# Kernel optimization log

Measured on AMD Instinct MI355X. Metric: run time of the kernel, lower is better.

The kernel has to match this reference:

```python
import jax, jax.numpy as jnp
import numpy as np
from jax import lax

GRAVITY = 9.8
DT = 0.1
MAX_STEPS = 200


def _conv(x, w, b):
    # x: [N,C,H,W], w: [O,I,3,3] (PyTorch OIHW), padding=1 -> SAME
    y = lax.conv_general_dilated(x, w, window_strides=(1, 1), padding='SAME',
                                 dimension_numbers=('NCHW', 'OIHW', 'NCHW'))
    return y + b[None, :, None, None]


def _maxpool2(x):
    return lax.reduce_window(x, -jnp.inf, lax.max,
                             window_dimensions=(1, 1, 2, 2),
                             window_strides=(1, 1, 2, 2), padding='VALID')


def setup_inputs() -> dict:
    key = jax.random.key(0)
    ks = jax.random.split(key, 12)
    B = 256
    x = jax.random.normal(ks[0], (B, 12, 128, 128), dtype=jnp.float32)

    def he(k, shape, fan_in):
        return jax.random.normal(k, shape, dtype=jnp.float32) * np.float32(np.sqrt(2.0 / fan_in))

    w1 = he(ks[1], (32, 12, 3, 3), 12 * 9); b1 = jnp.zeros((32,), jnp.float32)
    w2 = he(ks[2], (64, 32, 3, 3), 32 * 9); b2 = jnp.zeros((64,), jnp.float32)
    w3 = he(ks[3], (64, 64, 3, 3), 64 * 9); b3 = jnp.zeros((64,), jnp.float32)
    w4 = he(ks[4], (64, 64, 3, 3), 64 * 9); b4 = jnp.zeros((64,), jnp.float32)
    wl1 = he(ks[5], (128, 64 * 8 * 8), 64 * 8 * 8); bl1 = jnp.zeros((128,), jnp.float32)
    wl2 = he(ks[6], (4, 128), 128); bl2 = jnp.zeros((4,), jnp.float32)
    return {'x': x, 'w1': w1, 'b1': b1, 'w2': w2, 'b2': b2, 'w3': w3, 'b3': b3,
            'w4': w4, 'b4': b4, 'wl1': wl1, 'bl1': bl1, 'wl2': wl2, 'bl2': bl2}


def _forward(x, w1, b1, w2, b2, w3, b3, w4, b4, wl1, bl1, wl2, bl2):
    h = _maxpool2(jax.nn.relu(_conv(x, w1, b1)))   # [B,32,64,64]
    h = _maxpool2(jax.nn.relu(_conv(h, w2, b2)))   # [B,64,32,32]
    h = _maxpool2(jax.nn.relu(_conv(h, w3, b3)))   # [B,64,16,16]
    h = _maxpool2(jax.nn.relu(_conv(h, w4, b4)))   # [B,64,8,8]
    h = h.reshape(h.shape[0], -1)                  # [B,4096]
    h = jax.nn.relu(h @ wl1.T + bl1)               # [B,128]
    state = h @ wl2.T + bl2                        # [B,4]

    px, py, vx, vy = state[:, 0], state[:, 1], state[:, 2], state[:, 3]

    def step(carry, _):
        cx, cy, cvy = carry
        nvy = cvy - GRAVITY * DT
        nx = cx + vx * DT
        ny = jnp.maximum(cy + nvy * DT, 0.0)
        return (nx, ny, nvy), None

    (fx, _, _), _ = lax.scan(step, (px, py, vy), None, length=MAX_STEPS)
    return fx


def reference(x, w1, b1, w2, b2, w3, b3, w4, b4, wl1, bl1, wl2, bl2):
    return _forward(x, w1, b1, w2, b2, w3, b3, w4, b4, wl1, bl1, wl2, bl2)
```

## Files before the change

kernel.cpp:

```cpp
#include <hip/hip_runtime.h>


typedef _Float16 f16;
typedef _Float16 f16x8 __attribute__((ext_vector_type(8)));
typedef _Float16 f16x4 __attribute__((ext_vector_type(4)));
typedef float f32x4 __attribute__((ext_vector_type(4)));
typedef float f32x16 __attribute__((ext_vector_type(16)));

__global__ __launch_bounds__(512)
void pack_weights(const float* __restrict__ w1, const float* __restrict__ w2,
                  const float* __restrict__ w3, const float* __restrict__ w4,
                  f16* __restrict__ apack) {
  int idx = blockIdx.x * 512 + threadIdx.x;
  int frag = idx >> 9;
  int e = idx & 511;
  int lane = e >> 3, j = e & 7;
  float v = 0.f;
  if (frag < 9) {
    int kh = frag / 3, kw = frag % 3;
    int oc = lane & 31;
    int ic = (lane >> 5) * 8 + j;
    if (ic < 12) v = w1[((oc * 12 + ic) * 3 + kh) * 3 + kw];
  } else if (frag < 45) {
    int f = frag - 9;
    int sh = f >> 2, og = f & 3;
    int kh = sh / 3, kw = sh % 3;
    int row16 = lane & 15, kg = lane >> 4;
    int oc = og * 16 + row16;
    int ic = kg * 8 + j;
    v = w2[((oc * 32 + ic) * 3 + kh) * 3 + kw];
  } else {
    const float* w = (frag < 117) ? w3 : w4;
    int f = frag - ((frag < 117) ? 45 : 117);
    int sk = f >> 2, og = f & 3;
    int sh = sk >> 1, ks = sk & 1;
    int kh = sh / 3, kw = sh % 3;
    int row16 = lane & 15, kg = lane >> 4;
    int oc = og * 16 + row16;
    int ic = ks * 32 + kg * 8 + j;
    v = w[((oc * 64 + ic) * 3 + kh) * 3 + kw];
  }
  apack[idx] = (f16)v;
}

__global__ __launch_bounds__(512)
void conv1_mfma(const float* __restrict__ x, const f16* __restrict__ apack,
                const float* __restrict__ bias, f16* __restrict__ hout) {
  constexpr int W = 128, H = 128;
  constexpr int SR = 6, PADB = 48, ROWB = 130 * PADB;
  __shared__ char smem[SR * ROWB];
  const int tid = threadIdx.x;
  const int n = blockIdx.y;
  const int r0 = blockIdx.x * 4;

  if (tid < 36) {
    int slot = tid / 6, r = tid % 6;
    int px = (r >= 3) ? 129 : 0;
    int ch = r % 3;
    *(float4*)(smem + slot * ROWB + px * PADB + ch * 16) =
        make_float4(0.f, 0.f, 0.f, 0.f);
  }
  {
    const int g = tid >> 4;
    const int l16 = tid & 15;
    const int Q = l16 >> 2, q = l16 & 3;
    float4 a[SR];
#pragma unroll
    for (int sr = 0; sr < SR; ++sr) {
      const int ri = r0 + sr - 1;
      a[sr] = make_float4(0.f, 0.f, 0.f, 0.f);
      if (l16 < 12 && ri >= 0 && ri < H)
        a[sr] = *(const float4*)(x + ((size_t)(n * 12 + l16) * H + ri) * W + g * 4);
    }
#pragma unroll
    for (int sr = 0; sr < SR; ++sr) {
      float4 t1, t2;
      {
        float sx = __shfl_xor(a[sr].x, 1), sy = __shfl_xor(a[sr].y, 1);
        float sz = __shfl_xor(a[sr].z, 1), sw = __shfl_xor(a[sr].w, 1);
        bool odd = q & 1;
        t1.x = odd ? sy : a[sr].x;  t1.y = odd ? a[sr].y : sx;
        t1.z = odd ? sw : a[sr].z;  t1.w = odd ? a[sr].w : sz;
      }
      {
        float sx = __shfl_xor(t1.x, 2), sy = __shfl_xor(t1.y, 2);
        float sz = __shfl_xor(t1.z, 2), sw = __shfl_xor(t1.w, 2);
        bool hi = q & 2;
        t2.x = hi ? sz : t1.x;  t2.y = hi ? sw : t1.y;
        t2.z = hi ? t1.z : sx;  t2.w = hi ? t1.w : sy;
      }
      f16x4 h = { (f16)t2.x, (f16)t2.y, (f16)t2.z, (f16)t2.w };
      *(f16x4*)(smem + sr * ROWB + (g * 4 + q + 1) * PADB + Q * 8) = h;
    }
  }
  __syncthreads();

  const int wv = tid >> 6, l = tid & 63;
  const int rp = wv >> 2;
  const int pxb = (wv & 3) * 32;
  const int rl0 = rp * 2;
  const int ln = l & 31;
  const int hi = l >> 5;

  f16x8 A[9];
#pragma unroll
  for (int ks = 0; ks < 9; ++ks)
    A[ks] = *(const f16x8*)(apack + ((ks << 9) + (l << 3)));

  f32x16 acc[2];
  acc[0] = (f32x16)0.f;
  acc[1] = (f32x16)0.f;

#pragma unroll
  for (int rowi = 0; rowi < 2; ++rowi) {
#pragma unroll
    for (int ks = 0; ks < 9; ++ks) {
      const int kh = ks / 3, kw = ks % 3;
      const int slot = rl0 + rowi + kh;
      f16x8 B = *(const f16x8*)(smem + slot * ROWB + (pxb + ln + kw) * PADB + hi * 16);
      acc[rowi] = __builtin_amdgcn_mfma_f32_32x32x16_f16(A[ks], B, acc[rowi], 0, 0, 0);
    }
  }
  const int pr = blockIdx.x * 2 + rp;
#pragma unroll
  for (int g = 0; g < 4; ++g) {
    float v[4];
#pragma unroll
    for (int c = 0; c < 4; ++c) {
      float m = fmaxf(acc[0][g * 4 + c], acc[1][g * 4 + c]);
      v[c] = fmaxf(m, __shfl_xor(m, 1));
    }
    if ((l & 1) == 0) {
      const int pw = (pxb + ln) >> 1;
      const int oc0 = g * 8 + hi * 4;
      f16x4 pk;
#pragma unroll
      for (int c = 0; c < 4; ++c)
        pk[c] = (f16)fmaxf(v[c] + bias[oc0 + c], 0.f);
      *(f16x4*)(hout + (((size_t)(n * 64 + pr) * 64 + pw) * 32 + oc0)) = pk;
    }
  }
}

template<int C, int W, int H, int BR, int KS, int PADB, int PGn, bool NCHW_OUT>
__global__ __launch_bounds__(256)
void conv_shift(const f16* __restrict__ hin, const f16* __restrict__ apack,
                const float* __restrict__ bias, void* __restrict__ hout) {
  constexpr int SR = BR + 2;
  constexpr int ROWB = (W + 2) * PADB;
  __shared__ char smem[SR * ROWB];
  const int tid = threadIdx.x;
  const int n = blockIdx.y;
  const int r0 = blockIdx.x * BR;
  constexpr int CPC = C / 8;
  constexpr int TOTC = SR * (W + 2) * CPC;
  constexpr int NITER = (TOTC + 255) / 256;
  {
    float4 stg[NITER];
#pragma unroll
    for (int it = 0; it < NITER; ++it) {
      const int t = tid + it * 256;
      float4 v = make_float4(0.f, 0.f, 0.f, 0.f);
      if (t < TOTC) {
        int sr = t / ((W + 2) * CPC);
        int rem = t - sr * ((W + 2) * CPC);
        int px = rem / CPC;
        int kc = rem - px * CPC;
        int ri = r0 + sr - 1;
        int gx = px - 1;
        if (ri >= 0 && ri < H && gx >= 0 && gx < W)
          v = *(const float4*)(hin + (((size_t)(n * H + ri) * W + gx) * C + kc * 8));
      }
      stg[it] = v;
    }
#pragma unroll
    for (int it = 0; it < NITER; ++it) {
      const int t = tid + it * 256;
      if (t < TOTC) {
        int sr = t / ((W + 2) * CPC);
        int rem = t - sr * ((W + 2) * CPC);
        int px = rem / CPC;
        int kc = rem - px * CPC;
        *(float4*)(smem + sr * ROWB + px * PADB + kc * 16) = stg[it];
      }
    }
  }
  __syncthreads();

  const int wv = tid >> 6, l = tid & 63;
  constexpr int WPP = W / (16 * PGn);
  const int rp = wv / WPP;
  const int pxb = (wv % WPP) * 16 * PGn;
  const int rl0 = rp * 2;
  const int lp = l & 15, kg = l >> 4;
  const int px0 = pxb + lp;

  f32x4 acc[2][PGn][4];
#pragma unroll
  for (int a = 0; a < 2; ++a)
#pragma unroll
    for (int b = 0; b < PGn; ++b)
#pragma unroll
      for (int c = 0; c < 4; ++c)
        acc[a][b][c] = (f32x4){0.f, 0.f, 0.f, 0.f};

  for (int sh = 0; sh < 9; ++sh) {
    const int kh = sh / 3, kw = sh % 3;
    f16x8 A[KS][4];
#pragma unroll
    for (int ks = 0; ks < KS; ++ks)
#pragma unroll
      for (int og = 0; og < 4; ++og)
        A[ks][og] = *(const f16x8*)(apack + ((((sh * KS + ks) * 4 + og) << 9) + (l << 3)));
#pragma unroll
    for (int rowi = 0; rowi < 2; ++rowi) {
      const char* base = smem + (rl0 + rowi + kh) * ROWB;
#pragma unroll
      for (int pg = 0; pg < PGn; ++pg) {
#pragma unroll
        for (int ks = 0; ks < KS; ++ks) {
          f16x8 B = *(const f16x8*)(base + (px0 + pg * 16 + kw) * PADB + ks * 64 + kg * 16);
#pragma unroll
          for (int og = 0; og < 4; ++og)
            acc[rowi][pg][og] =
                __builtin_amdgcn_mfma_f32_16x16x32_f16(A[ks][og], B, acc[rowi][pg][og], 0, 0, 0);
        }
      }
    }
  }
  constexpr int PH = H / 2, PW = W / 2;
  const int pr = blockIdx.x * (BR / 2) + rp;
#pragma unroll
  for (int pg = 0; pg < PGn; ++pg) {
#pragma unroll
    for (int og = 0; og < 4; ++og) {
      float v[4];
#pragma unroll
      for (int c = 0; c < 4; ++c) {
        float m = fmaxf(acc[0][pg][og][c], acc[1][pg][og][c]);
        v[c] = fmaxf(m, __shfl_xor(m, 1));
      }
      if ((l & 1) == 0) {
        const int pw = (pxb + pg * 16 + lp) >> 1;
        const int oc0 = og * 16 + kg * 4;
        if constexpr (NCHW_OUT) {
          float* o = (float*)hout;
#pragma unroll
          for (int c = 0; c < 4; ++c)
            o[(((size_t)n * 64 + oc0 + c) * PH + pr) * PW + pw] =
                fmaxf(v[c] + bias[oc0 + c], 0.f);
        } else {
          f16x4 pk;
#pragma unroll
          for (int c = 0; c < 4; ++c)
            pk[c] = (f16)fmaxf(v[c] + bias[oc0 + c], 0.f);
          *(f16x4*)((f16*)hout + (((size_t)(n * PH + pr) * PW + pw) * 64 + oc0)) = pk;
        }
      }
    }
  }
}

__global__ __launch_bounds__(1024)
void fc_head(const float* __restrict__ h4, const float* __restrict__ wl1,
             const float* __restrict__ bl1, const float* __restrict__ wl2,
             const float* __restrict__ bl2, float* __restrict__ out) {
  __shared__ float rows[2][4096];
  __shared__ float red[8 * 128 * 2];
  __shared__ float red2[2 * 128];
  const int tid = threadIdx.x;
  const int b0 = blockIdx.x * 2;
  {
    const float4* src = (const float4*)(h4 + (size_t)b0 * 4096);
    float4* dst = (float4*)rows;
    for (int t = tid; t < 2048; t += 1024) dst[t] = src[t];
  }
  __syncthreads();

  const int nn = tid & 127;
  const int ks = tid >> 7;
  const float4* wp = (const float4*)(wl1 + (size_t)nn * 4096 + ks * 512);
  const float4* x0 = (const float4*)(&rows[0][ks * 512]);
  const float4* x1 = (const float4*)(&rows[1][ks * 512]);
  float s0 = 0.f, s1 = 0.f;
#pragma unroll 8
  for (int i = 0; i < 128; ++i) {
    float4 w = wp[i], a = x0[i], b = x1[i];
    s0 = fmaf(w.x, a.x, fmaf(w.y, a.y, fmaf(w.z, a.z, fmaf(w.w, a.w, s0))));
    s1 = fmaf(w.x, b.x, fmaf(w.y, b.y, fmaf(w.z, b.z, fmaf(w.w, b.w, s1))));
  }
  red[(ks * 128 + nn) * 2 + 0] = s0;
  red[(ks * 128 + nn) * 2 + 1] = s1;
  __syncthreads();

  if (tid < 256) {
    const int r = tid >> 7, n2 = tid & 127;
    float h = bl1[n2];
#pragma unroll
    for (int k = 0; k < 8; ++k) h += red[(k * 128 + n2) * 2 + r];
    h = fmaxf(h, 0.f);
    red2[r * 128 + n2] = h * (wl2[n2] + 20.0f * wl2[256 + n2]);
  }
  __syncthreads();
#pragma unroll
  for (int s = 64; s > 0; s >>= 1) {
    if (tid < 2 * s) {
      int r = tid / s, i = tid - r * s;
      red2[r * 128 + i] += red2[r * 128 + i + s];
    }
    __syncthreads();
  }
  if (tid < 2) out[b0 + tid] = red2[tid * 128] + bl2[0] + 20.0f * bl2[2];
}

extern "C" void kernel_launch(void* const* d_in, const int* in_sizes, int n_in,
                              void* d_out, int out_size, void* d_ws, size_t ws_size,
                              hipStream_t stream) {
  const float* x   = (const float*)d_in[0];
  const float* w1  = (const float*)d_in[1];
  const float* b1  = (const float*)d_in[2];
  const float* w2  = (const float*)d_in[3];
  const float* b2  = (const float*)d_in[4];
  const float* w3  = (const float*)d_in[5];
  const float* b3  = (const float*)d_in[6];
  const float* w4  = (const float*)d_in[7];
  const float* b4  = (const float*)d_in[8];
  const float* wl1 = (const float*)d_in[9];
  const float* bl1 = (const float*)d_in[10];
  const float* wl2 = (const float*)d_in[11];
  const float* bl2 = (const float*)d_in[12];
  float* out = (float*)d_out;
  char* ws = (char*)d_ws;

  f16* apack = (f16*)ws;
  f16* h1 = (f16*)(ws + (1u << 20));
  f16* h2 = (f16*)(ws + 68157440u);
  f16* h3 = (f16*)(ws + 101711872u);
  float* h4 = (float*)(ws + 110100480u);

  pack_weights<<<189, 512, 0, stream>>>(w1, w2, w3, w4, apack);
  conv1_mfma<<<dim3(32, 256), 512, 0, stream>>>(x, apack, b1, h1);
  conv_shift<32, 64, 64, 4, 1, 64, 2, false><<<dim3(16, 256), 256, 0, stream>>>(
      h1, apack + 9 * 512, b2, (void*)h2);
  conv_shift<64, 32, 32, 8, 2, 144, 2, false><<<dim3(4, 256), 256, 0, stream>>>(
      h2, apack + 45 * 512, b3, (void*)h3);
  conv_shift<64, 16, 16, 8, 2, 144, 1, true><<<dim3(2, 256), 256, 0, stream>>>(
      h3, apack + 117 * 512, b4, (void*)h4);
  fc_head<<<128, 1024, 0, stream>>>(h4, wl1, bl1, wl2, bl2, out);
}
```

Before: 243.0 us.

## Make conv1 persistent over row tiles with double-buffered LDS staging

```diff
diff --git a/kernel.cpp b/kernel.cpp
--- a/kernel.cpp
+++ b/kernel.cpp
@@ -43,28 +43,32 @@
   apack[idx] = (f16)v;
 }
 
-__global__ __launch_bounds__(512)
+__global__ __launch_bounds__(512, 4)
 void conv1_mfma(const float* __restrict__ x, const f16* __restrict__ apack,
                 const float* __restrict__ bias, f16* __restrict__ hout) {
   constexpr int W = 128, H = 128;
   constexpr int SR = 6, PADB = 48, ROWB = 130 * PADB;
-  __shared__ char smem[SR * ROWB];
+  constexpr int TPB = 8;
+  __shared__ char smem[2][SR * ROWB];
   const int tid = threadIdx.x;
   const int n = blockIdx.y;
-  const int r0 = blockIdx.x * 4;
-
-  if (tid < 36) {
-    int slot = tid / 6, r = tid % 6;
+
+  if (tid < 72) {
+    int b = tid / 36, rem = tid % 36;
+    int slot = rem / 6, r = rem % 6;
     int px = (r >= 3) ? 129 : 0;
     int ch = r % 3;
-    *(float4*)(smem + slot * ROWB + px * PADB + ch * 16) =
+    *(float4*)(smem[b] + slot * ROWB + px * PADB + ch * 16) =
         make_float4(0.f, 0.f, 0.f, 0.f);
   }
-  {
-    const int g = tid >> 4;
-    const int l16 = tid & 15;
-    const int Q = l16 >> 2, q = l16 & 3;
-    float4 a[SR];
+
+  const int g = tid >> 4;
+  const int l16 = tid & 15;
+  const int Q = l16 >> 2, q = l16 & 3;
+  float4 a[SR];
+
+  auto load_tile = [&](int t) {
+    const int r0 = (blockIdx.x * TPB + t) * 4;
 #pragma unroll
     for (int sr = 0; sr < SR; ++sr) {
       const int ri = r0 + sr - 1;
@@ -72,6 +76,8 @@
       if (l16 < 12 && ri >= 0 && ri < H)
         a[sr] = *(const float4*)(x + ((size_t)(n * 12 + l16) * H + ri) * W + g * 4);
     }
+  };
+  auto write_tile = [&](char* buf) {
 #pragma unroll
     for (int sr = 0; sr < SR; ++sr) {
       float4 t1, t2;
@@ -85,15 +91,14 @@
       {
         float sx = __shfl_xor(t1.x, 2), sy = __shfl_xor(t1.y, 2);
         float sz = __shfl_xor(t1.z, 2), sw = __shfl_xor(t1.w, 2);
-        bool hi = q & 2;
-        t2.x = hi ? sz : t1.x;  t2.y = hi ? sw : t1.y;
-        t2.z = hi ? t1.z : sx;  t2.w = hi ? t1.w : sy;
+        bool hi2 = q & 2;
+        t2.x = hi2 ? sz : t1.x;  t2.y = hi2 ? sw : t1.y;
+        t2.z = hi2 ? t1.z : sx;  t2.w = hi2 ? t1.w : sy;
       }
       f16x4 h = { (f16)t2.x, (f16)t2.y, (f16)t2.z, (f16)t2.w };
-      *(f16x4*)(smem + sr * ROWB + (g * 4 + q + 1) * PADB + Q * 8) = h;
-    }
-  }
-  __syncthreads();
+      *(f16x4*)(buf + sr * ROWB + (g * 4 + q + 1) * PADB + Q * 8) = h;
+    }
+  };
 
   const int wv = tid >> 6, l = tid & 63;
   const int rp = wv >> 2;
@@ -107,37 +112,49 @@
   for (int ks = 0; ks < 9; ++ks)
     A[ks] = *(const f16x8*)(apack + ((ks << 9) + (l << 3)));
 
-  f32x16 acc[2];
-  acc[0] = (f32x16)0.f;
-  acc[1] = (f32x16)0.f;
-
-#pragma unroll
-  for (int rowi = 0; rowi < 2; ++rowi) {
+  auto compute = [&](const char* buf, int tg) {
+    f32x16 acc0 = (f32x16)0.f, acc1 = (f32x16)0.f;
 #pragma unroll
     for (int ks = 0; ks < 9; ++ks) {
       const int kh = ks / 3, kw = ks % 3;
-      const int slot = rl0 + rowi + kh;
-      f16x8 B = *(const f16x8*)(smem + slot * ROWB + (pxb + ln + kw) * PADB + hi * 16);
-      acc[rowi] = __builtin_amdgcn_mfma_f32_32x32x16_f16(A[ks], B, acc[rowi], 0, 0, 0);
-    }
-  }
-  const int pr = blockIdx.x * 2 + rp;
-#pragma unroll
-  for (int g = 0; g < 4; ++g) {
-    float v[4];
-#pragma unroll
-    for (int c = 0; c < 4; ++c) {
-      float m = fmaxf(acc[0][g * 4 + c], acc[1][g * 4 + c]);
-      v[c] = fmaxf(m, __shfl_xor(m, 1));
-    }
-    if ((l & 1) == 0) {
-      const int pw = (pxb + ln) >> 1;
-      const int oc0 = g * 8 + hi * 4;
-      f16x4 pk;
-#pragma unroll
-      for (int c = 0; c < 4; ++c)
-        pk[c] = (f16)fmaxf(v[c] + bias[oc0 + c], 0.f);
-      *(f16x4*)(hout + (((size_t)(n * 64 + pr) * 64 + pw) * 32 + oc0)) = pk;
+      const char* base = buf + (pxb + ln + kw) * PADB + hi * 16;
+      f16x8 B0 = *(const f16x8*)(base + (rl0 + kh) * ROWB);
+      acc0 = __builtin_amdgcn_mfma_f32_32x32x16_f16(A[ks], B0, acc0, 0, 0, 0);
+      f16x8 B1 = *(const f16x8*)(base + (rl0 + 1 + kh) * ROWB);
+      acc1 = __builtin_amdgcn_mfma_f32_32x32x16_f16(A[ks], B1, acc1, 0, 0, 0);
+    }
+    const int pr = tg * 2 + rp;
+#pragma unroll
+    for (int gg = 0; gg < 4; ++gg) {
+      float v[4];
+#pragma unroll
+      for (int c = 0; c < 4; ++c) {
+        float m = fmaxf(acc0[gg * 4 + c], acc1[gg * 4 + c]);
+        v[c] = fmaxf(m, __shfl_xor(m, 1));
+      }
+      if ((l & 1) == 0) {
+        const int pw = (pxb + ln) >> 1;
+        const int oc0 = gg * 8 + hi * 4;
+        f16x4 pk;
+#pragma unroll
+        for (int c = 0; c < 4; ++c)
+          pk[c] = (f16)fmaxf(v[c] + bias[oc0 + c], 0.f);
+        *(f16x4*)(hout + (((size_t)(n * 64 + pr) * 64 + pw) * 32 + oc0)) = pk;
+      }
+    }
+  };
+
+  load_tile(0);
+  write_tile(smem[0]);
+  __syncthreads();
+
+  for (int t = 0; t < TPB; ++t) {
+    if (t + 1 < TPB) load_tile(t + 1);
+    compute(smem[t & 1], blockIdx.x * TPB + t);
+    __syncthreads();
+    if (t + 1 < TPB) {
+      write_tile(smem[(t + 1) & 1]);
+      __syncthreads();
     }
   }
 }
@@ -204,6 +221,7 @@
       for (int c = 0; c < 4; ++c)
         acc[a][b][c] = (f32x4){0.f, 0.f, 0.f, 0.f};
 
+#pragma unroll
   for (int sh = 0; sh < 9; ++sh) {
     const int kh = sh / 3, kw = sh % 3;
     f16x8 A[KS][4];
@@ -339,8 +357,8 @@
   float* h4 = (float*)(ws + 110100480u);
 
   pack_weights<<<189, 512, 0, stream>>>(w1, w2, w3, w4, apack);
-  conv1_mfma<<<dim3(32, 256), 512, 0, stream>>>(x, apack, b1, h1);
-  conv_shift<32, 64, 64, 4, 1, 64, 2, false><<<dim3(16, 256), 256, 0, stream>>>(
+  conv1_mfma<<<dim3(4, 256), 512, 0, stream>>>(x, apack, b1, h1);
+  conv_shift<32, 64, 64, 4, 1, 80, 2, false><<<dim3(16, 256), 256, 0, stream>>>(
       h1, apack + 9 * 512, b2, (void*)h2);
   conv_shift<64, 32, 32, 8, 2, 144, 2, false><<<dim3(4, 256), 256, 0, stream>>>(
       h2, apack + 45 * 512, b3, (void*)h3);
```

After: 246.3 us. Within noise of the previous version (+1.4%).
